# Optimization experiments

Hardware: AMD Instinct MI355X
Metric: run time of the kernel (lower is better)

Reference implementation:

```python
import jax, jax.numpy as jnp
import numpy as np

B, T, I, H, K = 32, 1024, 512, 512, 2


def _causal_conv1d(x_bit, w_hik, b_h):
    # x_bit: [B, I, T]; left-pad K-1 zeros (ConstantPad1d((K-1, 0)))
    xp = jnp.pad(x_bit, ((0, 0), (0, 0), (K - 1, 0)))
    y = jax.lax.conv_general_dilated(
        xp, w_hik, window_strides=(1,), padding='VALID',
        dimension_numbers=('NCH', 'OIH', 'NCH'))  # [B, H, T]
    return y + b_h[None, :, None]


def setup_inputs() -> dict:
    key = jax.random.key(0)
    k1, k2, k3 = jax.random.split(key, 3)
    bound = 1.0 / np.sqrt(I * K)  # torch Conv1d default init scale
    return {
        'inputs': jax.random.normal(k1, (B, T, I), dtype=jnp.float32),
        'init_state': jnp.zeros((B, H), dtype=jnp.float32),
        'Wz': jax.random.uniform(k2, (H, I, K), jnp.float32, -bound, bound),
        'bz': jnp.zeros((H,), dtype=jnp.float32),
        'Wf': jax.random.uniform(k3, (H, I, K), jnp.float32, -bound, bound),
        'bf': jnp.zeros((H,), dtype=jnp.float32),
    }


def reference(inputs, init_state, Wz, bz, Wf, bf):
    # init_state is accepted but unused in the original forward (mode='f').
    x = inputs.transpose(0, 2, 1)                      # [B, I, T]
    raw_f = _causal_conv1d(x, Wf, bf).transpose(0, 2, 1)  # [B, T, H]
    raw_z = _causal_conv1d(x, Wz, bz).transpose(0, 2, 1)  # [B, T, H]

    log_f = jax.nn.log_sigmoid(raw_f)
    log_one_minus_f = jax.nn.log_sigmoid(-raw_f)
    log_z = jax.nn.log_sigmoid(raw_z)

    # recurrent_gates[t] = sum_{s>t} log_f[s]  (suffix sum of log_f over time, excluding t=0 shift)
    rg = log_f[:, 1:, :]                               # [B, T-1, H]
    cs = jnp.cumsum(rg, axis=1)
    rg = rg - cs + cs[:, -1:, :]
    rg = jnp.concatenate([rg, jnp.zeros((inputs.shape[0], 1, rg.shape[2]), dtype=rg.dtype)], axis=1)  # [B, T, H]

    log_hidden = jax.lax.cumlogsumexp(log_z + log_one_minus_f + rg, axis=1)
    hidden = jnp.exp(log_hidden - rg)
    return hidden
```

## Files before the change

kernel.cpp:

```cpp
#include <hip/hip_runtime.h>
#include <hip/hip_bf16.h>
#include <cstddef>
#include <cstdint>

#define B_  32
#define T_  1024
#define I_  512
#define H_  512
#define M_  (B_ * T_)
#define TP_ 1025

typedef __bf16 bf16x8  __attribute__((ext_vector_type(8)));
typedef float  floatx4 __attribute__((ext_vector_type(4)));
typedef unsigned short ushort8v __attribute__((ext_vector_type(8)));
typedef unsigned long long u64;

__device__ __forceinline__ unsigned short f2bf(float f) {
    uint32_t u = __float_as_uint(f);
    return (unsigned short)((u + 0x7FFFu + ((u >> 16) & 1u)) >> 16);
}
__device__ __forceinline__ float sigm(float x) {
    return __builtin_amdgcn_rcpf(1.f + __expf(-x));
}

#define GLL(src, dst) __builtin_amdgcn_global_load_lds( \
    (const __attribute__((address_space(1))) void*)(src), \
    (__attribute__((address_space(3))) void*)(dst), 16, 0, 0)

#define NB_BUILD 8200
#define NB_PACK  512

__global__ __launch_bounds__(256) void prep(const float* __restrict__ x,
                                            const float* __restrict__ Wf,
                                            const float* __restrict__ Wz,
                                            unsigned short* __restrict__ Ab2,
                                            unsigned short* __restrict__ Wp) {
    if (blockIdx.x < NB_BUILD) {
        int g = blockIdx.x * 256 + threadIdx.x;
        int idx8 = g << 3;
        int row = idx8 >> 9;
        int col = idx8 & 511;
        int b    = (int)((unsigned)row / TP_);
        int trow = row - b * TP_;
        ushort8v o = {0, 0, 0, 0, 0, 0, 0, 0};
        if (trow > 0) {
            const float* src = &x[((size_t)b * T_ + (trow - 1)) * I_ + col];
            float4 v0 = *(const float4*)src;
            float4 v1 = *(const float4*)(src + 4);
            o[0] = f2bf(v0.x); o[1] = f2bf(v0.y); o[2] = f2bf(v0.z); o[3] = f2bf(v0.w);
            o[4] = f2bf(v1.x); o[5] = f2bf(v1.y); o[6] = f2bf(v1.z); o[7] = f2bf(v1.w);
        }
        *(ushort8v*)&Ab2[(size_t)idx8] = o;
    } else {
        int g = (blockIdx.x - NB_BUILD) * 256 + threadIdx.x;
        int e8   = g << 3;
        int gate = e8 >> 19;
        int e2   = e8 & 524287;
        int ksub = e2 >> 14;
        int h    = (e2 >> 5) & 511;
        int kw0  = e2 & 31;
        const float* G = gate ? Wz : Wf;
        ushort8v o;
        #pragma unroll
        for (int j = 0; j < 8; ++j) {
            int kk  = ksub * 32 + kw0 + j;
            int tap = kk >> 9;
            int i   = kk & 511;
            o[j] = f2bf(G[h * (I_ * 2) + i * 2 + tap]);
        }
        *(ushort8v*)&Wp[(size_t)e8] = o;
    }
}

__global__ __launch_bounds__(256, 2) void mfma_gemm_scan(
        const unsigned short* __restrict__ Ab2,
        const unsigned short* __restrict__ Wp,
        const float* __restrict__ biasF,
        const float* __restrict__ biasZ,
        float* __restrict__ out,
        u64* __restrict__ Hpub,
        uint32_t* __restrict__ counter) {
    __shared__ unsigned short smem[24576];
    __shared__ uint32_t vid_s;

    const int tid = threadIdx.x;
    if (tid == 0) vid_s = atomicAdd(counter, 1u);
    __syncthreads();
    const int vid   = (int)vid_s;
    const int pos   = vid >> 7;
    const int chain = vid & 127;
    const int b     = chain & 31;
    const int ni    = chain >> 5;
    const int h0    = ni * 128;
    const int browBase = b * TP_ + pos * 128;

    const int lane = tid & 63;
    const int wave = tid >> 6;
    const int wm   = wave >> 1, wn = wave & 1;
    const int lm   = lane & 15, quad = lane >> 4;

    const int c0 = wave * 128 + lane;
    const int c1 = c0 + 64;
    const int r0 = c0 >> 2, q0 = (c0 & 3) ^ ((r0 >> 2) & 3);
    const int r1 = c1 >> 2, q1 = (c1 & 3) ^ ((r1 >> 2) & 3);

    const unsigned short* WpF = Wp;
    const unsigned short* WpZ = Wp + 524288;

    const unsigned short* pA0 = Ab2 + (size_t)(browBase + r0) * 512 + q0 * 8;
    const unsigned short* pA1 = Ab2 + (size_t)(browBase + r1) * 512 + q1 * 8;
    const unsigned short* pF0 = WpF + (size_t)(h0 + r0) * 32 + q0 * 8;
    const unsigned short* pF1 = WpF + (size_t)(h0 + r1) * 32 + q1 * 8;
    const unsigned short* pZ0 = WpZ + (size_t)(h0 + r0) * 32 + q0 * 8;
    const unsigned short* pZ1 = WpZ + (size_t)(h0 + r1) * 32 + q1 * 8;

    unsigned short* dA0 = smem + wave * 1024;
    unsigned short* dA1 = smem + wave * 1024 + 512;
    unsigned short* dF0 = smem + 4096 + wave * 1024;
    unsigned short* dF1 = smem + 4096 + wave * 1024 + 512;
    unsigned short* dZ0 = smem + 8192 + wave * 1024;
    unsigned short* dZ1 = smem + 8192 + wave * 1024 + 512;

    int offA[4], offB[4];
    #pragma unroll
    for (int r = 0; r < 4; ++r) {
        int ml = wm * 64 + r * 16 + lm;
        offA[r] = (4 * ml + (quad ^ ((ml >> 2) & 3))) * 8;
    }
    #pragma unroll
    for (int c = 0; c < 4; ++c) {
        int nl = wn * 64 + c * 16 + lm;
        offB[c] = 4096 + (4 * nl + (quad ^ ((nl >> 2) & 3))) * 8;
    }

    floatx4 accF[4][4] = {};
    floatx4 accZ[4][4] = {};

    for (int kt2 = 0; kt2 < 16; ++kt2) {
        const int tap = kt2 >> 3;
        const int i0  = (kt2 & 7) * 64;
        #pragma unroll
        for (int s = 0; s < 2; ++s) {
            const int aoff = tap * 512 + i0 + s * 32;
            const size_t woff = (size_t)(kt2 * 2 + s) * 16384;
            const int ls = s * 12288;
            GLL(pA0 + aoff, dA0 + ls);
            GLL(pA1 + aoff, dA1 + ls);
            GLL(pF0 + woff, dF0 + ls);
            GLL(pF1 + woff, dF1 + ls);
            GLL(pZ0 + woff, dZ0 + ls);
            GLL(pZ1 + woff, dZ1 + ls);
        }
        __syncthreads();

        #pragma unroll
        for (int s = 0; s < 2; ++s) {
            const int ls = s * 12288;
            bf16x8 af[4], bF[4], bZ[4];
            #pragma unroll
            for (int r = 0; r < 4; ++r) af[r] = *(const bf16x8*)(smem + ls + offA[r]);
            #pragma unroll
            for (int c = 0; c < 4; ++c) {
                bF[c] = *(const bf16x8*)(smem + ls + offB[c]);
                bZ[c] = *(const bf16x8*)(smem + ls + offB[c] + 4096);
            }
            #pragma unroll
            for (int r = 0; r < 4; ++r) {
                #pragma unroll
                for (int c = 0; c < 4; ++c) {
                    accF[r][c] = __builtin_amdgcn_mfma_f32_16x16x32_bf16(
                                    af[r], bF[c], accF[r][c], 0, 0, 0);
                    accZ[r][c] = __builtin_amdgcn_mfma_f32_16x16x32_bf16(
                                    af[r], bZ[c], accZ[r][c], 0, 0, 0);
                }
            }
        }
        __syncthreads();
    }

    float bfv[4], bzv[4];
    #pragma unroll
    for (int c = 0; c < 4; ++c) {
        int hc = h0 + wn * 64 + c * 16 + lm;
        bfv[c] = biasF[hc];
        bzv[c] = biasZ[hc];
    }

    float2* seg  = (float2*)smem;
    float*  hinL = (float*)&smem[16384];

    #pragma unroll
    for (int r = 0; r < 4; ++r) {
        const int sid = wm * 16 + r * 4 + quad;
        #pragma unroll
        for (int c = 0; c < 4; ++c) {
            float A = 1.f, C = 0.f;
            #pragma unroll
            for (int v = 0; v < 4; ++v) {
                float f = sigm(accF[r][c][v] + bfv[c]);
                float z = sigm(accZ[r][c][v] + bzv[c]);
                accF[r][c][v] = f;
                accZ[r][c][v] = z;
                A *= f;
                C = fmaf(f, C - z, z);
            }
            seg[sid * 128 + wn * 64 + c * 16 + lm] = make_float2(A, C);
        }
    }
    __syncthreads();

    float Hin = 0.f;
    if (tid < 128) {
        float At = 1.f, Ct = 0.f;
        #pragma unroll 8
        for (int s = 0; s < 32; ++s) {
            float2 sc = seg[s * 128 + tid];
            Ct = fmaf(sc.x, Ct, sc.y);
            At *= sc.x;
        }
        if (pos > 0) {
            u64* p = &Hpub[((size_t)(pos - 1) * 128 + chain) * 128 + tid];
            u64 v;
            while (((v = atomicAdd(p, 0ull)) >> 32) == 0ull)
                __builtin_amdgcn_s_sleep(2);
            Hin = __uint_as_float((uint32_t)v);
        }
        if (pos < 7) {
            float Hout = fmaf(At, Hin, Ct);
            u64 pv = 0x100000000ull | (u64)__float_as_uint(Hout);
            atomicExch(&Hpub[((size_t)pos * 128 + chain) * 128 + tid], pv);
        }
        float run = Hin;
        #pragma unroll 8
        for (int s = 0; s < 32; ++s) {
            hinL[s * 128 + tid] = run;
            float2 sc = seg[s * 128 + tid];
            run = fmaf(sc.x, run, sc.y);
        }
    }
    __syncthreads();

    const int rowBase = b * T_ + pos * 128;
    #pragma unroll
    for (int r = 0; r < 4; ++r) {
        const int sid = wm * 16 + r * 4 + quad;
        #pragma unroll
        for (int c = 0; c < 4; ++c) {
            const int hc = h0 + wn * 64 + c * 16 + lm;
            float hs = hinL[sid * 128 + (hc - h0)];
            #pragma unroll
            for (int v = 0; v < 4; ++v) {
                float f = accF[r][c][v];
                float z = accZ[r][c][v];
                hs = fmaf(f, hs - z, z);
                const size_t row = (size_t)(rowBase + wm * 64 + r * 16 + quad * 4 + v);
                out[row * H_ + hc] = hs;
            }
        }
    }
}

extern "C" void kernel_launch(void* const* d_in, const int* in_sizes, int n_in,
                              void* d_out, int out_size, void* d_ws, size_t ws_size,
                              hipStream_t stream) {
    const float* x  = (const float*)d_in[0];
    const float* Wz = (const float*)d_in[2];
    const float* bz = (const float*)d_in[3];
    const float* Wf = (const float*)d_in[4];
    const float* bf = (const float*)d_in[5];
    float* out = (float*)d_out;

    char* ws = (char*)d_ws;
    unsigned short* Ab2  = (unsigned short*)(ws);
    unsigned short* Wp   = (unsigned short*)(ws + (size_t)34 * 1024 * 1024);
    u64*            Hpub = (u64*)(ws + (size_t)36 * 1024 * 1024);
    uint32_t*       cnt  = (uint32_t*)(ws + (size_t)37 * 1024 * 1024);

    hipMemsetAsync(Hpub, 0, (size_t)1024 * 1024 + 4096, stream);

    prep<<<NB_BUILD + NB_PACK, 256, 0, stream>>>(x, Wf, Wz, Ab2, Wp);

    mfma_gemm_scan<<<1024, 256, 0, stream>>>(Ab2, Wp, bf, bz, out, Hpub, cnt);
}
```

Baseline: 203.2 us.

## Load weight fragments directly from global in MFMA layout; fold memset into prep

```diff
diff --git a/kernel.cpp b/kernel.cpp
--- a/kernel.cpp
+++ b/kernel.cpp
@@ -29,12 +29,15 @@
 
 #define NB_BUILD 8200
 #define NB_PACK  512
+#define NB_ZERO  256
 
 __global__ __launch_bounds__(256) void prep(const float* __restrict__ x,
                                             const float* __restrict__ Wf,
                                             const float* __restrict__ Wz,
                                             unsigned short* __restrict__ Ab2,
-                                            unsigned short* __restrict__ Wp) {
+                                            unsigned short* __restrict__ Wq,
+                                            uint4* __restrict__ HpubZ,
+                                            uint32_t* __restrict__ cnt) {
     if (blockIdx.x < NB_BUILD) {
         int g = blockIdx.x * 256 + threadIdx.x;
         int idx8 = g << 3;
@@ -51,30 +54,35 @@
             o[4] = f2bf(v1.x); o[5] = f2bf(v1.y); o[6] = f2bf(v1.z); o[7] = f2bf(v1.w);
         }
         *(ushort8v*)&Ab2[(size_t)idx8] = o;
-    } else {
-        int g = (blockIdx.x - NB_BUILD) * 256 + threadIdx.x;
-        int e8   = g << 3;
-        int gate = e8 >> 19;
-        int e2   = e8 & 524287;
-        int ksub = e2 >> 14;
-        int h    = (e2 >> 5) & 511;
-        int kw0  = e2 & 31;
+    } else if (blockIdx.x < NB_BUILD + NB_PACK) {
+        int cid = (blockIdx.x - NB_BUILD) * 256 + threadIdx.x;
+        int lane = cid & 63;
+        int c    = (cid >> 6) & 3;
+        int wn   = (cid >> 8) & 1;
+        int ksub = (cid >> 9) & 31;
+        int ni   = (cid >> 14) & 3;
+        int gate = (cid >> 16) & 1;
+        int n_col = ni * 128 + wn * 64 + c * 16 + (lane & 15);
         const float* G = gate ? Wz : Wf;
         ushort8v o;
         #pragma unroll
         for (int j = 0; j < 8; ++j) {
-            int kk  = ksub * 32 + kw0 + j;
-            int tap = kk >> 9;
-            int i   = kk & 511;
-            o[j] = f2bf(G[h * (I_ * 2) + i * 2 + tap]);
-        }
-        *(ushort8v*)&Wp[(size_t)e8] = o;
+            int k   = ksub * 32 + (lane >> 4) * 8 + j;
+            int tap = k >> 9;
+            int i   = k & 511;
+            o[j] = f2bf(G[n_col * (I_ * 2) + i * 2 + tap]);
+        }
+        *(ushort8v*)&Wq[(size_t)cid * 8] = o;
+    } else {
+        int g = (blockIdx.x - NB_BUILD - NB_PACK) * 256 + threadIdx.x;
+        HpubZ[g] = make_uint4(0, 0, 0, 0);
+        if (g == 0) *cnt = 0;
     }
 }
 
 __global__ __launch_bounds__(256, 2) void mfma_gemm_scan(
         const unsigned short* __restrict__ Ab2,
-        const unsigned short* __restrict__ Wp,
+        const unsigned short* __restrict__ Wq,
         const float* __restrict__ biasF,
         const float* __restrict__ biasZ,
         float* __restrict__ out,
@@ -104,34 +112,20 @@
     const int r0 = c0 >> 2, q0 = (c0 & 3) ^ ((r0 >> 2) & 3);
     const int r1 = c1 >> 2, q1 = (c1 & 3) ^ ((r1 >> 2) & 3);
 
-    const unsigned short* WpF = Wp;
-    const unsigned short* WpZ = Wp + 524288;
-
     const unsigned short* pA0 = Ab2 + (size_t)(browBase + r0) * 512 + q0 * 8;
     const unsigned short* pA1 = Ab2 + (size_t)(browBase + r1) * 512 + q1 * 8;
-    const unsigned short* pF0 = WpF + (size_t)(h0 + r0) * 32 + q0 * 8;
-    const unsigned short* pF1 = WpF + (size_t)(h0 + r1) * 32 + q1 * 8;
-    const unsigned short* pZ0 = WpZ + (size_t)(h0 + r0) * 32 + q0 * 8;
-    const unsigned short* pZ1 = WpZ + (size_t)(h0 + r1) * 32 + q1 * 8;
 
     unsigned short* dA0 = smem + wave * 1024;
     unsigned short* dA1 = smem + wave * 1024 + 512;
-    unsigned short* dF0 = smem + 4096 + wave * 1024;
-    unsigned short* dF1 = smem + 4096 + wave * 1024 + 512;
-    unsigned short* dZ0 = smem + 8192 + wave * 1024;
-    unsigned short* dZ1 = smem + 8192 + wave * 1024 + 512;
-
-    int offA[4], offB[4];
+
+    const unsigned short* wq = Wq + ni * 131072 + wn * 2048 + lane * 8;
+
+    int offA[4];
     #pragma unroll
     for (int r = 0; r < 4; ++r) {
         int ml = wm * 64 + r * 16 + lm;
         offA[r] = (4 * ml + (quad ^ ((ml >> 2) & 3))) * 8;
     }
-    #pragma unroll
-    for (int c = 0; c < 4; ++c) {
-        int nl = wn * 64 + c * 16 + lm;
-        offB[c] = 4096 + (4 * nl + (quad ^ ((nl >> 2) & 3))) * 8;
-    }
 
     floatx4 accF[4][4] = {};
     floatx4 accZ[4][4] = {};
@@ -142,28 +136,23 @@
         #pragma unroll
         for (int s = 0; s < 2; ++s) {
             const int aoff = tap * 512 + i0 + s * 32;
-            const size_t woff = (size_t)(kt2 * 2 + s) * 16384;
-            const int ls = s * 12288;
-            GLL(pA0 + aoff, dA0 + ls);
-            GLL(pA1 + aoff, dA1 + ls);
-            GLL(pF0 + woff, dF0 + ls);
-            GLL(pF1 + woff, dF1 + ls);
-            GLL(pZ0 + woff, dZ0 + ls);
-            GLL(pZ1 + woff, dZ1 + ls);
+            GLL(pA0 + aoff, dA0 + s * 4096);
+            GLL(pA1 + aoff, dA1 + s * 4096);
         }
         __syncthreads();
 
         #pragma unroll
         for (int s = 0; s < 2; ++s) {
-            const int ls = s * 12288;
+            const int ksub = kt2 * 2 + s;
+            const unsigned short* wqk = wq + ksub * 4096;
             bf16x8 af[4], bF[4], bZ[4];
             #pragma unroll
-            for (int r = 0; r < 4; ++r) af[r] = *(const bf16x8*)(smem + ls + offA[r]);
-            #pragma unroll
             for (int c = 0; c < 4; ++c) {
-                bF[c] = *(const bf16x8*)(smem + ls + offB[c]);
-                bZ[c] = *(const bf16x8*)(smem + ls + offB[c] + 4096);
-            }
+                bF[c] = *(const bf16x8*)(wqk + c * 512);
+                bZ[c] = *(const bf16x8*)(wqk + 524288 + c * 512);
+            }
+            #pragma unroll
+            for (int r = 0; r < 4; ++r) af[r] = *(const bf16x8*)(smem + s * 4096 + offA[r]);
             #pragma unroll
             for (int r = 0; r < 4; ++r) {
                 #pragma unroll
@@ -272,13 +261,12 @@
 
     char* ws = (char*)d_ws;
     unsigned short* Ab2  = (unsigned short*)(ws);
-    unsigned short* Wp   = (unsigned short*)(ws + (size_t)34 * 1024 * 1024);
+    unsigned short* Wq   = (unsigned short*)(ws + (size_t)34 * 1024 * 1024);
     u64*            Hpub = (u64*)(ws + (size_t)36 * 1024 * 1024);
     uint32_t*       cnt  = (uint32_t*)(ws + (size_t)37 * 1024 * 1024);
 
-    hipMemsetAsync(Hpub, 0, (size_t)1024 * 1024 + 4096, stream);
-
-    prep<<<NB_BUILD + NB_PACK, 256, 0, stream>>>(x, Wf, Wz, Ab2, Wp);
-
-    mfma_gemm_scan<<<1024, 256, 0, stream>>>(Ab2, Wp, bf, bz, out, Hpub, cnt);
-}
+    prep<<<NB_BUILD + NB_PACK + NB_ZERO, 256, 0, stream>>>(
+        x, Wf, Wz, Ab2, Wq, (uint4*)Hpub, cnt);
+
+    mfma_gemm_scan<<<1024, 256, 0, stream>>>(Ab2, Wq, bf, bz, out, Hpub, cnt);
+}
```

Result: slower. 208.0 us (+2.4%).
